# Performance work log

Measured on AMD Instinct MI355X. Metric: run time of the kernel, lower is better.

## Reference

```python
import jax, jax.numpy as jnp
import numpy as np

N = 20000      # nodes
E = 640000     # edges (before self-loops)
NFEAT = 512
NHID = 128
HEADS = 2
NOUT = 64
K = 100
ALPHA = 0.2          # LeakyReLU negative slope
CLUSTER_TEMP = 5.0


def gat_layer(x, W, a_src, a_dst, b, src, dst, n, heads, out_c, neg_slope):
    """PyG-style GATConv (eval mode, self-loops already in src/dst).
    W: [heads*out_c, in_c], a_src/a_dst: [heads, out_c], b: [heads*out_c]."""
    h = (x @ W.T).reshape(n, heads, out_c)               # [N,H,C]
    alpha_src = (h * a_src[None]).sum(-1)                # [N,H]
    alpha_dst = (h * a_dst[None]).sum(-1)                # [N,H]
    e = alpha_src[src] + alpha_dst[dst]                  # [E',H]
    e = jnp.where(e > 0, e, neg_slope * e)               # LeakyReLU
    # segment softmax over incoming edges of each dst node
    m = jax.ops.segment_max(e, dst, num_segments=n)
    ex = jnp.exp(e - m[dst])
    s = jax.ops.segment_sum(ex, dst, num_segments=n)
    a = ex / (s[dst] + 1e-16)                            # [E',H]
    out = jax.ops.segment_sum(h[src] * a[:, :, None], dst, num_segments=n)
    return out.reshape(n, heads * out_c) + b


def cluster_iter(data_n, mu, num_iter, cluster_temp):
    """Soft k-means on row-normalized data. data_n: [N,D], mu: [K,D]."""
    def body(mu, _):
        dist = data_n @ mu.T                              # [N,K]
        r = jax.nn.softmax(cluster_temp * dist, axis=1)
        cluster_r = r.sum(axis=0)                         # [K]
        cluster_mean = r.T @ data_n                       # [K,D]
        return cluster_mean / cluster_r[:, None], None
    mu, _ = jax.lax.scan(body, mu, None, length=num_iter)
    dist = data_n @ mu.T
    r = jax.nn.softmax(cluster_temp * dist, axis=1)
    return mu, r, dist


def setup_inputs() -> dict:
    key = jax.random.key(0)
    ks = jax.random.split(key, 12)
    x = jax.random.normal(ks[0], (N, NFEAT), dtype=jnp.float32)
    edge_index = jax.random.randint(ks[1], (2, E), 0, N, dtype=jnp.int32)
    # GATConv layer 1 params
    W1 = jax.random.normal(ks[2], (HEADS * NHID, NFEAT), dtype=jnp.float32) * 0.05
    a_src1 = jax.random.normal(ks[3], (HEADS, NHID), dtype=jnp.float32) * 0.1
    a_dst1 = jax.random.normal(ks[4], (HEADS, NHID), dtype=jnp.float32) * 0.1
    b1 = jnp.zeros((HEADS * NHID,), dtype=jnp.float32)
    # GATConv layer 2 params (heads=1)
    W2 = jax.random.normal(ks[5], (NOUT, HEADS * NHID), dtype=jnp.float32) * 0.05
    a_src2 = jax.random.normal(ks[6], (1, NOUT), dtype=jnp.float32) * 0.1
    a_dst2 = jax.random.normal(ks[7], (1, NOUT), dtype=jnp.float32) * 0.1
    b2 = jnp.zeros((NOUT,), dtype=jnp.float32)
    # cluster init (self.init = torch.rand(K, nout))
    mu0 = jax.random.uniform(ks[8], (K, NOUT), dtype=jnp.float32)
    return {"x": x, "W1": W1, "a_src1": a_src1, "a_dst1": a_dst1, "b1": b1,
            "W2": W2, "a_src2": a_src2, "a_dst2": a_dst2, "b2": b2,
            "mu0": mu0, "edge_index": edge_index, "num_iter": 10}


def reference(x, W1, a_src1, a_dst1, b1, W2, a_src2, a_dst2, b2, mu0,
              edge_index, num_iter):
    loops = jnp.arange(N, dtype=edge_index.dtype)
    src = jnp.concatenate([edge_index[0], loops])
    dst = jnp.concatenate([edge_index[1], loops])
    h = jax.nn.elu(gat_layer(x, W1, a_src1, a_dst1, b1, src, dst,
                             N, HEADS, NHID, ALPHA))
    embeds = gat_layer(h, W2, a_src2, a_dst2, b2, src, dst,
                       N, 1, NOUT, ALPHA) + 1e-6
    data_n = embeds / jnp.linalg.norm(embeds, axis=1, keepdims=True)
    mu_init, _, _ = cluster_iter(data_n, mu0, num_iter, CLUSTER_TEMP)
    mu, r, dist = cluster_iter(data_n, jax.lax.stop_gradient(mu_init), 1,
                               CLUSTER_TEMP)
    return mu, r, embeds, dist
```

## Files before the change

kernel.cpp:

```cpp
#include <hip/hip_runtime.h>
#include <hip/hip_bf16.h>
#include <math.h>

#define Nn 20000
#define Ee 640000
#define ETOT 660000
#define NF 512
#define C1 256
#define C2 64
#define KC 100
#define TEMP 5.0f
#define NSLOPE 0.2f
#define NPB 500
#define CHB 40

typedef __attribute__((ext_vector_type(8))) short bf16x8;
typedef __attribute__((ext_vector_type(4))) float f32x4;

__device__ __forceinline__ float wredSum(float v) {
#pragma unroll
  for (int off = 32; off > 0; off >>= 1) v += __shfl_xor(v, off, 64);
  return v;
}
__device__ __forceinline__ ushort f2bf(float f) {
  __hip_bfloat16 b = __float2bfloat16(f);
  return *(ushort*)&b;
}
__device__ __forceinline__ float bf2f(ushort u) {
  __hip_bfloat16 b = *(__hip_bfloat16*)&u;
  return __bfloat162float(b);
}

__global__ void hist_kernel(const int* __restrict__ ei, int* __restrict__ deg) {
  int e = blockIdx.x * 256 + threadIdx.x;
  if (e >= ETOT) return;
  int dst = e < Ee ? ei[Ee + e] : e - Ee;
  atomicAdd(&deg[dst], 1);
}

__global__ __launch_bounds__(1024) void scan2_kernel(const int* __restrict__ deg,
    int* __restrict__ rowp, int* __restrict__ curs) {
  __shared__ int wsum[16];
  __shared__ int wpre[16];
  int t = threadIdx.x;
  int lane = t & 63, w = t >> 6;
  int loc[20];
  int tot = 0;
  int base = t * 20;
  if (t < 1000) {
#pragma unroll
    for (int i = 0; i < 20; i++) { tot += deg[base + i]; loc[i] = tot; }
  }
  int s = tot;
#pragma unroll
  for (int off = 1; off < 64; off <<= 1) {
    int u = __shfl_up(s, off, 64);
    if (lane >= off) s += u;
  }
  if (lane == 63) wsum[w] = s;
  __syncthreads();
  if (t == 0) {
    int c = 0;
#pragma unroll
    for (int i = 0; i < 16; i++) { c += wsum[i]; wpre[i] = c; }
    rowp[0] = 0;
  }
  __syncthreads();
  int p = (w > 0 ? wpre[w - 1] : 0) + s - tot;
  if (t < 1000) {
    int prev = 0;
#pragma unroll
    for (int i = 0; i < 20; i++) {
      rowp[base + i + 1] = p + loc[i];
      curs[base + i] = p + prev;
      prev = loc[i];
    }
  }
}

__global__ void scatter_kernel(const int* __restrict__ ei, int* __restrict__ curs,
                               int* __restrict__ ssort, int* __restrict__ dsort) {
  int e = blockIdx.x * 256 + threadIdx.x;
  if (e >= ETOT) return;
  int src = e < Ee ? ei[e] : e - Ee;
  int dst = e < Ee ? ei[Ee + e] : e - Ee;
  int pos = atomicAdd(&curs[dst], 1);
  ssort[pos] = src;
  dsort[pos] = dst;
}

__global__ __launch_bounds__(256) void edge_e1(const int* __restrict__ ssort,
    const int* __restrict__ dsort, const float* __restrict__ asn,
    const float* __restrict__ adn, float2* __restrict__ eb) {
  int i = blockIdx.x * 256 + threadIdx.x;
  if (i >= ETOT) return;
  int s = ssort[i], d = dsort[i];
  float2 a = ((const float2*)asn)[s];
  float2 b = ((const float2*)adn)[d];
  float e0 = a.x + b.x, e1 = a.y + b.y;
  e0 = e0 > 0.f ? e0 : NSLOPE * e0;
  e1 = e1 > 0.f ? e1 : NSLOPE * e1;
  eb[i] = make_float2(e0, e1);
}

__global__ __launch_bounds__(256) void edge_e2(const int* __restrict__ ssort,
    const int* __restrict__ dsort, const float* __restrict__ asn,
    const float* __restrict__ adn, float* __restrict__ eb) {
  int i = blockIdx.x * 256 + threadIdx.x;
  if (i >= ETOT) return;
  float e = asn[ssort[i]] + adn[dsort[i]];
  eb[i] = e > 0.f ? e : NSLOPE * e;
}

__global__ __launch_bounds__(256) void gemm1_mfma(const float* __restrict__ A,
    const float* __restrict__ B, float* __restrict__ C) {
  __shared__ ushort Ah[128 * 40], Al[128 * 40], Bh[128 * 40], Bl[128 * 40];
  int tid = threadIdx.x;
  int bm = blockIdx.x << 7, bn = blockIdx.y << 7;
  int w = tid >> 6, lane = tid & 63;
  int wm = (w >> 1) << 6, wn = (w & 1) << 6;
  int fr = lane & 15, ko = (lane >> 4) << 3;
  f32x4 acc[4][4] = {};
  for (int k0 = 0; k0 < 512; k0 += 32) {
    __syncthreads();
#pragma unroll
    for (int cc = 0; cc < 4; cc++) {
      int c = tid + (cc << 8);
      int row = c >> 3, q = c & 7;
      int off = row * 40 + (q << 2);
      int gr = bm + row;
      float4 va = (gr < Nn) ? *(const float4*)(A + (size_t)gr * NF + k0 + (q << 2))
                            : make_float4(0.f, 0.f, 0.f, 0.f);
      float4 vb = *(const float4*)(B + (size_t)(bn + row) * NF + k0 + (q << 2));
      ushort h0 = f2bf(va.x), h1 = f2bf(va.y), h2 = f2bf(va.z), h3 = f2bf(va.w);
      *(ushort4*)&Ah[off] = make_ushort4(h0, h1, h2, h3);
      *(ushort4*)&Al[off] = make_ushort4(
          f2bf(va.x - bf2f(h0)), f2bf(va.y - bf2f(h1)),
          f2bf(va.z - bf2f(h2)), f2bf(va.w - bf2f(h3)));
      ushort g0 = f2bf(vb.x), g1 = f2bf(vb.y), g2 = f2bf(vb.z), g3 = f2bf(vb.w);
      *(ushort4*)&Bh[off] = make_ushort4(g0, g1, g2, g3);
      *(ushort4*)&Bl[off] = make_ushort4(
          f2bf(vb.x - bf2f(g0)), f2bf(vb.y - bf2f(g1)),
          f2bf(vb.z - bf2f(g2)), f2bf(vb.w - bf2f(g3)));
    }
    __syncthreads();
    bf16x8 aH[4], bH[4], t[4];
#pragma unroll
    for (int mf = 0; mf < 4; mf++)
      aH[mf] = *(const bf16x8*)&Ah[(wm + (mf << 4) + fr) * 40 + ko];
#pragma unroll
    for (int nf = 0; nf < 4; nf++)
      bH[nf] = *(const bf16x8*)&Bh[(wn + (nf << 4) + fr) * 40 + ko];
#pragma unroll
    for (int mf = 0; mf < 4; mf++)
#pragma unroll
      for (int nf = 0; nf < 4; nf++)
        acc[mf][nf] = __builtin_amdgcn_mfma_f32_16x16x32_bf16(aH[mf], bH[nf], acc[mf][nf], 0, 0, 0);
#pragma unroll
    for (int nf = 0; nf < 4; nf++)
      t[nf] = *(const bf16x8*)&Bl[(wn + (nf << 4) + fr) * 40 + ko];
#pragma unroll
    for (int mf = 0; mf < 4; mf++)
#pragma unroll
      for (int nf = 0; nf < 4; nf++)
        acc[mf][nf] = __builtin_amdgcn_mfma_f32_16x16x32_bf16(aH[mf], t[nf], acc[mf][nf], 0, 0, 0);
#pragma unroll
    for (int mf = 0; mf < 4; mf++)
      t[mf] = *(const bf16x8*)&Al[(wm + (mf << 4) + fr) * 40 + ko];
#pragma unroll
    for (int mf = 0; mf < 4; mf++)
#pragma unroll
      for (int nf = 0; nf < 4; nf++)
        acc[mf][nf] = __builtin_amdgcn_mfma_f32_16x16x32_bf16(t[mf], bH[nf], acc[mf][nf], 0, 0, 0);
  }
  int cr = (lane >> 4) << 2, cc2 = lane & 15;
#pragma unroll
  for (int mf = 0; mf < 4; mf++) {
#pragma unroll
    for (int r = 0; r < 4; r++) {
      int row = bm + wm + (mf << 4) + cr + r;
      if (row < Nn) {
#pragma unroll
        for (int nf = 0; nf < 4; nf++)
          C[(size_t)row * C1 + bn + wn + (nf << 4) + cc2] = acc[mf][nf][r];
      }
    }
  }
}

__global__ __launch_bounds__(256) void gemm_nt(const float* __restrict__ A,
    const float* __restrict__ B, float* __restrict__ C, int M, int N, int K) {
  __shared__ __align__(16) float As[16][68];
  __shared__ __align__(16) float Bs[16][68];
  int tid = threadIdx.x;
  int bm = blockIdx.x << 6, bn = blockIdx.y << 6;
  int lr = tid >> 2;
  int lc = (tid & 3) << 2;
  int tx = tid & 15, ty = tid >> 4;
  float acc[4][4] = {};
  for (int k0 = 0; k0 < K; k0 += 16) {
    int am = bm + lr;
    float4 av = make_float4(0.f, 0.f, 0.f, 0.f);
    if (am < M) av = *(const float4*)(A + (size_t)am * K + k0 + lc);
    float4 bv = *(const float4*)(B + (size_t)(bn + lr) * K + k0 + lc);
    __syncthreads();
    As[lc + 0][lr] = av.x; As[lc + 1][lr] = av.y; As[lc + 2][lr] = av.z; As[lc + 3][lr] = av.w;
    Bs[lc + 0][lr] = bv.x; Bs[lc + 1][lr] = bv.y; Bs[lc + 2][lr] = bv.z; Bs[lc + 3][lr] = bv.w;
    __syncthreads();
#pragma unroll
    for (int k = 0; k < 16; k++) {
      float4 a = *(const float4*)&As[k][ty << 2];
      float4 b = *(const float4*)&Bs[k][tx << 2];
      float aa[4] = {a.x, a.y, a.z, a.w};
      float bb[4] = {b.x, b.y, b.z, b.w};
#pragma unroll
      for (int i = 0; i < 4; i++)
#pragma unroll
        for (int j = 0; j < 4; j++) acc[i][j] += aa[i] * bb[j];
    }
  }
#pragma unroll
  for (int i = 0; i < 4; i++) {
    int row = bm + (ty << 2) + i;
    if (row < M) {
#pragma unroll
      for (int j = 0; j < 4; j++)
        C[(size_t)row * N + bn + (tx << 2) + j] = acc[i][j];
    }
  }
}

__global__ __launch_bounds__(256) void alpha1_kernel(const float* __restrict__ h,
    const float* __restrict__ a_src, const float* __restrict__ a_dst,
    float* __restrict__ asn, float* __restrict__ adn) {
  int l = threadIdx.x & 63;
  int n = (blockIdx.x << 2) + (threadIdx.x >> 6);
  if (n >= Nn) return;
  const float* hr = h + (size_t)n * C1;
  float h0 = hr[l], h1v = hr[64 + l], h2v = hr[128 + l], h3v = hr[192 + l];
  float ps0 = h0 * a_src[l] + h1v * a_src[64 + l];
  float pd0 = h0 * a_dst[l] + h1v * a_dst[64 + l];
  float ps1 = h2v * a_src[128 + l] + h3v * a_src[192 + l];
  float pd1 = h2v * a_dst[128 + l] + h3v * a_dst[192 + l];
  ps0 = wredSum(ps0); pd0 = wredSum(pd0); ps1 = wredSum(ps1); pd1 = wredSum(pd1);
  if (l == 0) {
    asn[2 * n] = ps0; asn[2 * n + 1] = ps1;
    adn[2 * n] = pd0; adn[2 * n + 1] = pd1;
  }
}

__global__ __launch_bounds__(256) void alpha2_kernel(const float* __restrict__ h,
    const float* __restrict__ a_src, const float* __restrict__ a_dst,
    float* __restrict__ asn, float* __restrict__ adn) {
  int l = threadIdx.x & 63;
  int n = (blockIdx.x << 2) + (threadIdx.x >> 6);
  if (n >= Nn) return;
  float v = h[(size_t)n * C2 + l];
  float ps = wredSum(v * a_src[l]);
  float pd = wredSum(v * a_dst[l]);
  if (l == 0) { asn[n] = ps; adn[n] = pd; }
}

__global__ __launch_bounds__(256) void agg1_kernel(const float* __restrict__ h,
    const float2* __restrict__ eb, const int* __restrict__ ssort,
    const float* __restrict__ b1, const int* __restrict__ rowp,
    float* __restrict__ ho) {
  __shared__ float redm[8], reds[8];
  __shared__ __align__(16) float slab[4][256];
  int n = blockIdx.x, tid = threadIdx.x;
  int w = tid >> 6, l = tid & 63;
  int lo = rowp[n], hi = rowp[n + 1];
  float m0 = -1e30f, s0 = 0.f, m1 = -1e30f, s1 = 0.f;
  for (int i = lo + tid; i < hi; i += 256) {
    float2 e = eb[i];
    if (e.x > m0) { s0 = s0 * __expf(m0 - e.x) + 1.f; m0 = e.x; }
    else s0 += __expf(e.x - m0);
    if (e.y > m1) { s1 = s1 * __expf(m1 - e.y) + 1.f; m1 = e.y; }
    else s1 += __expf(e.y - m1);
  }
#pragma unroll
  for (int off = 32; off > 0; off >>= 1) {
    float om = __shfl_xor(m0, off, 64), os = __shfl_xor(s0, off, 64);
    float nm = fmaxf(m0, om);
    s0 = s0 * __expf(m0 - nm) + os * __expf(om - nm); m0 = nm;
    om = __shfl_xor(m1, off, 64); os = __shfl_xor(s1, off, 64);
    nm = fmaxf(m1, om);
    s1 = s1 * __expf(m1 - nm) + os * __expf(om - nm); m1 = nm;
  }
  if (l == 0) { redm[w] = m0; reds[w] = s0; redm[4 + w] = m1; reds[4 + w] = s1; }
  __syncthreads();
  float M0 = fmaxf(fmaxf(redm[0], redm[1]), fmaxf(redm[2], redm[3]));
  float M1 = fmaxf(fmaxf(redm[4], redm[5]), fmaxf(redm[6], redm[7]));
  float S0 = reds[0] * __expf(redm[0] - M0) + reds[1] * __expf(redm[1] - M0)
           + reds[2] * __expf(redm[2] - M0) + reds[3] * __expf(redm[3] - M0);
  float S1 = reds[4] * __expf(redm[4] - M1) + reds[5] * __expf(redm[5] - M1)
           + reds[6] * __expf(redm[6] - M1) + reds[7] * __expf(redm[7] - M1);
  float inv0 = 1.f / (S0 + 1e-16f), inv1 = 1.f / (S1 + 1e-16f);
  const bool lo_head = (l < 32);
  float Msel = lo_head ? M0 : M1;
  float isel = lo_head ? inv0 : inv1;
  int ch = l << 2;
  int deg = hi - lo;
  float4 accA = {0.f, 0.f, 0.f, 0.f}, accB = {0.f, 0.f, 0.f, 0.f};
  int j = w;
  for (; j + 4 < deg; j += 8) {
    int i0 = lo + j, i1 = lo + j + 4;
    float2 eA = eb[i0];
    float2 eB = eb[i1];
    int sA = ssort[i0], sB = ssort[i1];
    float4 ha = *(const float4*)(h + (size_t)sA * C1 + ch);
    float4 hb = *(const float4*)(h + (size_t)sB * C1 + ch);
    float wtA = __expf((lo_head ? eA.x : eA.y) - Msel) * isel;
    float wtB = __expf((lo_head ? eB.x : eB.y) - Msel) * isel;
    accA.x += wtA * ha.x; accA.y += wtA * ha.y; accA.z += wtA * ha.z; accA.w += wtA * ha.w;
    accB.x += wtB * hb.x; accB.y += wtB * hb.y; accB.z += wtB * hb.z; accB.w += wtB * hb.w;
  }
  if (j < deg) {
    int i0 = lo + j;
    float2 eA = eb[i0];
    int sA = ssort[i0];
    float4 ha = *(const float4*)(h + (size_t)sA * C1 + ch);
    float wtA = __expf((lo_head ? eA.x : eA.y) - Msel) * isel;
    accA.x += wtA * ha.x; accA.y += wtA * ha.y; accA.z += wtA * ha.z; accA.w += wtA * ha.w;
  }
  accA.x += accB.x; accA.y += accB.y; accA.z += accB.z; accA.w += accB.w;
  *(float4*)&slab[w][ch] = accA;
  __syncthreads();
  float v = slab[0][tid] + slab[1][tid] + slab[2][tid] + slab[3][tid] + b1[tid];
  ho[(size_t)n * C1 + tid] = v > 0.f ? v : __expf(v) - 1.0f;
}

__global__ __launch_bounds__(256) void agg2_kernel(const float* __restrict__ h,
    const float* __restrict__ eb, const int* __restrict__ ssort,
    const float* __restrict__ b2, const int* __restrict__ rowp,
    float* __restrict__ emb, float* __restrict__ dnrm) {
  int tid = threadIdx.x;
  int w = tid >> 6, l = tid & 63;
  int n = (blockIdx.x << 2) + w;
  int lo = rowp[n], hi = rowp[n + 1];
  float m = -1e30f, s = 0.f;
  for (int i = lo + l; i < hi; i += 64) {
    float e = eb[i];
    if (e > m) { s = s * __expf(m - e) + 1.f; m = e; }
    else s += __expf(e - m);
  }
#pragma unroll
  for (int off = 32; off > 0; off >>= 1) {
    float om = __shfl_xor(m, off, 64), os = __shfl_xor(s, off, 64);
    float nm = fmaxf(m, om);
    s = s * __expf(m - nm) + os * __expf(om - nm); m = nm;
  }
  float inv = 1.f / (s + 1e-16f);
  int g = l >> 4, lg = l & 15, ch = lg << 2;
  int deg = hi - lo;
  float4 accA = {0.f, 0.f, 0.f, 0.f}, accB = {0.f, 0.f, 0.f, 0.f};
  int j = g;
  for (; j + 4 < deg; j += 8) {
    int i0 = lo + j, i1 = lo + j + 4;
    float eA = eb[i0], eB = eb[i1];
    int sA = ssort[i0], sB = ssort[i1];
    float4 ha = *(const float4*)(h + (size_t)sA * C2 + ch);
    float4 hb = *(const float4*)(h + (size_t)sB * C2 + ch);
    float wtA = __expf(eA - m) * inv;
    float wtB = __expf(eB - m) * inv;
    accA.x += wtA * ha.x; accA.y += wtA * ha.y; accA.z += wtA * ha.z; accA.w += wtA * ha.w;
    accB.x += wtB * hb.x; accB.y += wtB * hb.y; accB.z += wtB * hb.z; accB.w += wtB * hb.w;
  }
  if (j < deg) {
    int i0 = lo + j;
    float eA = eb[i0];
    int sA = ssort[i0];
    float4 ha = *(const float4*)(h + (size_t)sA * C2 + ch);
    float wtA = __expf(eA - m) * inv;
    accA.x += wtA * ha.x; accA.y += wtA * ha.y; accA.z += wtA * ha.z; accA.w += wtA * ha.w;
  }
  accA.x += accB.x; accA.y += accB.y; accA.z += accB.z; accA.w += accB.w;
#pragma unroll
  for (int off = 16; off <= 32; off <<= 1) {
    accA.x += __shfl_xor(accA.x, off, 64);
    accA.y += __shfl_xor(accA.y, off, 64);
    accA.z += __shfl_xor(accA.z, off, 64);
    accA.w += __shfl_xor(accA.w, off, 64);
  }
  float4 bv = *(const float4*)(b2 + ch);
  float e0 = accA.x + bv.x + 1e-6f;
  float e1 = accA.y + bv.y + 1e-6f;
  float e2 = accA.z + bv.z + 1e-6f;
  float e3 = accA.w + bv.w + 1e-6f;
  float dot = e0 * e0 + e1 * e1 + e2 * e2 + e3 * e3;
#pragma unroll
  for (int off = 1; off < 16; off <<= 1) dot += __shfl_xor(dot, off, 64);
  float invn = 1.f / sqrtf(dot);
  if (g == 0) {
    *(float4*)(emb + (size_t)n * C2 + ch) = make_float4(e0, e1, e2, e3);
    *(float4*)(dnrm + (size_t)n * C2 + ch) =
        make_float4(e0 * invn, e1 * invn, e2 * invn, e3 * invn);
  }
}

template <int MODE>
__global__ __launch_bounds__(256) void fused_ac(
    const float* __restrict__ dnp, const float* __restrict__ mu_init,
    const float* __restrict__ mu, float* __restrict__ pcm, float* __restrict__ pcr,
    float* __restrict__ rout, float* __restrict__ distout,
    int it, const int* __restrict__ niter) {
  if (MODE == 0) { if (it > niter[0]) return; }
  __shared__ __align__(16) float mu_s[KC * 68];
  __shared__ __align__(16) float d_s[CHB * 64];
  __shared__ __align__(16) float r_s[CHB * KC];
  int tid = threadIdx.x, blk = blockIdx.x;
  const float* msrc = (MODE == 0 && it == 0) ? mu_init : mu;
  for (int idx = tid; idx < KC * 64; idx += 256)
    mu_s[(idx >> 6) * 68 + (idx & 63)] = msrc[idx];
  for (int idx = tid; idx < CHB * 64; idx += 256)
    d_s[idx] = dnp[(size_t)blk * (CHB * 64) + idx];
  __syncthreads();
  int w = tid >> 6, l = tid & 63;
  const bool has2 = l < (KC - 64);
  int l2 = has2 ? 64 + l : l;
  int nbase = w * 10;
  float z1[5][2] = {}, z2[5][2] = {};
#pragma unroll 4
  for (int dq = 0; dq < 16; dq++) {
    float4 m1 = *(const float4*)&mu_s[l * 68 + (dq << 2)];
    float4 m2 = *(const float4*)&mu_s[l2 * 68 + (dq << 2)];
#pragma unroll
    for (int g = 0; g < 5; g++) {
#pragma unroll
      for (int nb = 0; nb < 2; nb++) {
        float4 dv = *(const float4*)&d_s[(nbase + g * 2 + nb) * 64 + (dq << 2)];
        z1[g][nb] += m1.x * dv.x + m1.y * dv.y + m1.z * dv.z + m1.w * dv.w;
        z2[g][nb] += m2.x * dv.x + m2.y * dv.y + m2.z * dv.z + m2.w * dv.w;
      }
    }
  }
#pragma unroll
  for (int g = 0; g < 5; g++) {
#pragma unroll
    for (int nb = 0; nb < 2; nb++) {
      float e1 = __expf(TEMP * z1[g][nb]);
      float e2 = has2 ? __expf(TEMP * z2[g][nb]) : 0.f;
      float inv = 1.0f / wredSum(e1 + e2);
      int nl = nbase + g * 2 + nb;
      if (MODE == 0) {
        r_s[nl * KC + l] = e1 * inv;
        if (has2) r_s[nl * KC + 64 + l] = e2 * inv;
      } else {
        size_t n = (size_t)blk * CHB + nl;
        rout[n * KC + l] = e1 * inv;
        if (has2) rout[n * KC + 64 + l] = e2 * inv;
        distout[n * KC + l] = z1[g][nb];
        if (has2) distout[n * KC + 64 + l] = z2[g][nb];
      }
    }
  }
  if (MODE == 0) {
    __syncthreads();
    int tx = tid & 15, ky = tid >> 4;
    const bool two = (ky < 9);
    int kq0 = ky, kq1 = 16 + ky;
    float a0[4][4] = {}, a1[4][4] = {};
    float ar0[4] = {}, ar1[4] = {};
#pragma unroll 2
    for (int j = 0; j < CHB; j++) {
      float4 dv = *(const float4*)&d_s[j * 64 + (tx << 2)];
      float4 r0 = *(const float4*)&r_s[j * KC + (kq0 << 2)];
      float rv0[4] = {r0.x, r0.y, r0.z, r0.w};
#pragma unroll
      for (int i = 0; i < 4; i++) {
        a0[i][0] += rv0[i] * dv.x; a0[i][1] += rv0[i] * dv.y;
        a0[i][2] += rv0[i] * dv.z; a0[i][3] += rv0[i] * dv.w;
      }
      if (tx == 0) { ar0[0] += r0.x; ar0[1] += r0.y; ar0[2] += r0.z; ar0[3] += r0.w; }
      if (two) {
        float4 r1 = *(const float4*)&r_s[j * KC + (kq1 << 2)];
        float rv1[4] = {r1.x, r1.y, r1.z, r1.w};
#pragma unroll
        for (int i = 0; i < 4; i++) {
          a1[i][0] += rv1[i] * dv.x; a1[i][1] += rv1[i] * dv.y;
          a1[i][2] += rv1[i] * dv.z; a1[i][3] += rv1[i] * dv.w;
        }
        if (tx == 0) { ar1[0] += r1.x; ar1[1] += r1.y; ar1[2] += r1.z; ar1[3] += r1.w; }
      }
    }
#pragma unroll
    for (int i = 0; i < 4; i++) {
      *(float4*)&pcm[(size_t)blk * 6400 + (kq0 * 4 + i) * 64 + (tx << 2)] =
          make_float4(a0[i][0], a0[i][1], a0[i][2], a0[i][3]);
      if (two)
        *(float4*)&pcm[(size_t)blk * 6400 + (kq1 * 4 + i) * 64 + (tx << 2)] =
            make_float4(a1[i][0], a1[i][1], a1[i][2], a1[i][3]);
    }
    if (tx == 0) {
      *(float4*)&pcr[(size_t)blk * KC + kq0 * 4] = make_float4(ar0[0], ar0[1], ar0[2], ar0[3]);
      if (two)
        *(float4*)&pcr[(size_t)blk * KC + kq1 * 4] = make_float4(ar1[0], ar1[1], ar1[2], ar1[3]);
    }
  }
}

__global__ __launch_bounds__(256) void muupd_kernel(const float* __restrict__ pcm,
    const float* __restrict__ pcr, float* __restrict__ mu,
    int it, const int* __restrict__ niter) {
  if (it > niter[0]) return;
  __shared__ float part[4][64];
  __shared__ float redc[4];
  int k = blockIdx.x, tid = threadIdx.x;
  int d = tid & 63, bg = tid >> 6;
  float s = 0.f;
  for (int b = bg; b < NPB; b += 4)
    s += pcm[(size_t)b * 6400 + k * 64 + d];
  part[bg][d] = s;
  float c = 0.f;
  for (int b = tid; b < NPB; b += 256) c += pcr[b * KC + k];
  c = wredSum(c);
  if ((tid & 63) == 0) redc[tid >> 6] = c;
  __syncthreads();
  if (tid < 64) {
    float cr = redc[0] + redc[1] + redc[2] + redc[3];
    mu[k * 64 + tid] = (part[0][tid] + part[1][tid] + part[2][tid] + part[3][tid]) / cr;
  }
}

__global__ void copy_f(const float* __restrict__ a, float* __restrict__ b, int n) {
  int i = blockIdx.x * 256 + threadIdx.x;
  if (i < n) b[i] = a[i];
}

extern "C" void kernel_launch(void* const* d_in, const int* in_sizes, int n_in,
                              void* d_out, int out_size, void* d_ws, size_t ws_size,
                              hipStream_t stream) {
  const float* x    = (const float*)d_in[0];
  const float* W1   = (const float*)d_in[1];
  const float* asr1 = (const float*)d_in[2];
  const float* ads1 = (const float*)d_in[3];
  const float* b1   = (const float*)d_in[4];
  const float* W2   = (const float*)d_in[5];
  const float* asr2 = (const float*)d_in[6];
  const float* ads2 = (const float*)d_in[7];
  const float* b2   = (const float*)d_in[8];
  const float* mu0  = (const float*)d_in[9];
  const int*   ei   = (const int*)d_in[10];
  const int*   nit  = (const int*)d_in[11];

  float* f = (float*)d_ws;
  float* h1   = f;  f += (size_t)Nn * C1;
  float* h1o  = f;  f += (size_t)Nn * C1;
  float* as1  = f;  f += Nn * 2;
  float* ad1  = f;  f += Nn * 2;
  float* h2   = f;  f += (size_t)Nn * C2;
  float* as2  = f;  f += Nn;
  float* ad2  = f;  f += Nn;
  float* dn   = f;  f += (size_t)Nn * C2;
  float* mu   = f;  f += KC * C2;
  float2* ebA = (float2*)f; f += (size_t)ETOT * 2;
  float* ebB  = (float*)ebA;
  float* pcm  = h1;
  float* pcr  = h1 + (size_t)NPB * 6400;
  int* ip = (int*)f;
  int* deg   = ip;  ip += Nn;
  int* rowp  = ip;  ip += Nn + 1;
  int* curs  = ip;  ip += Nn;
  int* ssort = ip;  ip += ETOT;
  int* dsort = ip;  ip += ETOT;

  float* out_mu = (float*)d_out;
  float* out_r  = out_mu + KC * C2;
  float* out_e  = out_r + (size_t)Nn * KC;
  float* out_d  = out_e + (size_t)Nn * C2;

  hipMemsetAsync(deg, 0, Nn * sizeof(int), stream);
  hist_kernel<<<(ETOT + 255) / 256, 256, 0, stream>>>(ei, deg);
  scan2_kernel<<<1, 1024, 0, stream>>>(deg, rowp, curs);
  scatter_kernel<<<(ETOT + 255) / 256, 256, 0, stream>>>(ei, curs, ssort, dsort);

  gemm1_mfma<<<dim3(157, 2), 256, 0, stream>>>(x, W1, h1);
  alpha1_kernel<<<5000, 256, 0, stream>>>(h1, asr1, ads1, as1, ad1);
  edge_e1<<<(ETOT + 255) / 256, 256, 0, stream>>>(ssort, dsort, as1, ad1, ebA);
  agg1_kernel<<<Nn, 256, 0, stream>>>(h1, ebA, ssort, b1, rowp, h1o);

  gemm_nt<<<dim3(313, 1), 256, 0, stream>>>(h1o, W2, h2, Nn, C2, C1);
  alpha2_kernel<<<5000, 256, 0, stream>>>(h2, asr2, ads2, as2, ad2);
  edge_e2<<<(ETOT + 255) / 256, 256, 0, stream>>>(ssort, dsort, as2, ad2, ebB);
  agg2_kernel<<<5000, 256, 0, stream>>>(h2, ebB, ssort, b2, rowp, out_e, dn);

  for (int it = 0; it < 12; it++) {
    fused_ac<0><<<NPB, 256, 0, stream>>>(dn, mu0, mu, pcm, pcr, nullptr, nullptr, it, nit);
    muupd_kernel<<<KC, 256, 0, stream>>>(pcm, pcr, mu, it, nit);
  }
  fused_ac<1><<<NPB, 256, 0, stream>>>(dn, mu0, mu, nullptr, nullptr, out_r, out_d, 0, nit);
  copy_f<<<25, 256, 0, stream>>>(mu, out_mu, KC * C2);
}
```

Measured before the change: 1.053 ms.

## Replace per-block partials and mu-update kernel with atomic accumulation slabs

Each k-means iteration block now atomically adds its partial cluster sums and counts into a per-iteration slab, instead of writing them to a partial buffer that a separate muupd kernel reduces. The next iteration's kernel normalizes the previous slab while loading mu, so the 12 muupd launches and the final copy kernel are removed. This cuts launch count and the partial-buffer write and reread. In exchange, it adds heavy float atomic contention (500 blocks each adding 6400 values), a memset of the slabs, and a summation order that is no longer deterministic.

```diff
diff --git a/kernel.cpp b/kernel.cpp
--- a/kernel.cpp
+++ b/kernel.cpp
@@ -13,6 +13,7 @@
 #define NSLOPE 0.2f
 #define NPB 500
 #define CHB 40
+#define SLAB 6500
 
 typedef __attribute__((ext_vector_type(8))) short bf16x8;
 typedef __attribute__((ext_vector_type(4))) float f32x4;
@@ -401,17 +402,26 @@
 template <int MODE>
 __global__ __launch_bounds__(256) void fused_ac(
     const float* __restrict__ dnp, const float* __restrict__ mu_init,
-    const float* __restrict__ mu, float* __restrict__ pcm, float* __restrict__ pcr,
-    float* __restrict__ rout, float* __restrict__ distout,
+    float* __restrict__ muacc,
+    float* __restrict__ rout, float* __restrict__ distout, float* __restrict__ out_mu,
     int it, const int* __restrict__ niter) {
   if (MODE == 0) { if (it > niter[0]) return; }
   __shared__ __align__(16) float mu_s[KC * 68];
   __shared__ __align__(16) float d_s[CHB * 64];
   __shared__ __align__(16) float r_s[CHB * KC];
+  __shared__ float rcp_s[KC];
   int tid = threadIdx.x, blk = blockIdx.x;
-  const float* msrc = (MODE == 0 && it == 0) ? mu_init : mu;
-  for (int idx = tid; idx < KC * 64; idx += 256)
-    mu_s[(idx >> 6) * 68 + (idx & 63)] = msrc[idx];
+  int src_it = (MODE == 0) ? it - 1 : niter[0];
+  if (MODE == 0 && it == 0) {
+    for (int idx = tid; idx < KC * 64; idx += 256)
+      mu_s[(idx >> 6) * 68 + (idx & 63)] = mu_init[idx];
+  } else {
+    const float* acc_prev = muacc + (size_t)src_it * SLAB;
+    if (tid < KC) rcp_s[tid] = 1.0f / acc_prev[6400 + tid];
+    __syncthreads();
+    for (int idx = tid; idx < KC * 64; idx += 256)
+      mu_s[(idx >> 6) * 68 + (idx & 63)] = acc_prev[idx] * rcp_s[idx >> 6];
+  }
   for (int idx = tid; idx < CHB * 64; idx += 256)
     d_s[idx] = dnp[(size_t)blk * (CHB * 64) + idx];
   __syncthreads();
@@ -456,6 +466,7 @@
   }
   if (MODE == 0) {
     __syncthreads();
+    float* acc = muacc + (size_t)it * SLAB;
     int tx = tid & 15, ky = tid >> 4;
     const bool two = (ky < 9);
     int kq0 = ky, kq1 = 16 + ky;
@@ -485,46 +496,25 @@
     }
 #pragma unroll
     for (int i = 0; i < 4; i++) {
-      *(float4*)&pcm[(size_t)blk * 6400 + (kq0 * 4 + i) * 64 + (tx << 2)] =
-          make_float4(a0[i][0], a0[i][1], a0[i][2], a0[i][3]);
-      if (two)
-        *(float4*)&pcm[(size_t)blk * 6400 + (kq1 * 4 + i) * 64 + (tx << 2)] =
-            make_float4(a1[i][0], a1[i][1], a1[i][2], a1[i][3]);
+#pragma unroll
+      for (int q = 0; q < 4; q++) {
+        atomicAdd(&acc[(kq0 * 4 + i) * 64 + (tx << 2) + q], a0[i][q]);
+        if (two) atomicAdd(&acc[(kq1 * 4 + i) * 64 + (tx << 2) + q], a1[i][q]);
+      }
     }
     if (tx == 0) {
-      *(float4*)&pcr[(size_t)blk * KC + kq0 * 4] = make_float4(ar0[0], ar0[1], ar0[2], ar0[3]);
-      if (two)
-        *(float4*)&pcr[(size_t)blk * KC + kq1 * 4] = make_float4(ar1[0], ar1[1], ar1[2], ar1[3]);
-    }
-  }
-}
-
-__global__ __launch_bounds__(256) void muupd_kernel(const float* __restrict__ pcm,
-    const float* __restrict__ pcr, float* __restrict__ mu,
-    int it, const int* __restrict__ niter) {
-  if (it > niter[0]) return;
-  __shared__ float part[4][64];
-  __shared__ float redc[4];
-  int k = blockIdx.x, tid = threadIdx.x;
-  int d = tid & 63, bg = tid >> 6;
-  float s = 0.f;
-  for (int b = bg; b < NPB; b += 4)
-    s += pcm[(size_t)b * 6400 + k * 64 + d];
-  part[bg][d] = s;
-  float c = 0.f;
-  for (int b = tid; b < NPB; b += 256) c += pcr[b * KC + k];
-  c = wredSum(c);
-  if ((tid & 63) == 0) redc[tid >> 6] = c;
-  __syncthreads();
-  if (tid < 64) {
-    float cr = redc[0] + redc[1] + redc[2] + redc[3];
-    mu[k * 64 + tid] = (part[0][tid] + part[1][tid] + part[2][tid] + part[3][tid]) / cr;
-  }
-}
-
-__global__ void copy_f(const float* __restrict__ a, float* __restrict__ b, int n) {
-  int i = blockIdx.x * 256 + threadIdx.x;
-  if (i < n) b[i] = a[i];
+#pragma unroll
+      for (int i = 0; i < 4; i++) {
+        atomicAdd(&acc[6400 + kq0 * 4 + i], ar0[i]);
+        if (two) atomicAdd(&acc[6400 + kq1 * 4 + i], ar1[i]);
+      }
+    }
+  } else {
+    if (blk == 0) {
+      for (int idx = tid; idx < KC * 64; idx += 256)
+        out_mu[idx] = mu_s[(idx >> 6) * 68 + (idx & 63)];
+    }
+  }
 }
 
 extern "C" void kernel_launch(void* const* d_in, const int* in_sizes, int n_in,
@@ -544,19 +534,17 @@
   const int*   nit  = (const int*)d_in[11];
 
   float* f = (float*)d_ws;
-  float* h1   = f;  f += (size_t)Nn * C1;
-  float* h1o  = f;  f += (size_t)Nn * C1;
-  float* as1  = f;  f += Nn * 2;
-  float* ad1  = f;  f += Nn * 2;
-  float* h2   = f;  f += (size_t)Nn * C2;
-  float* as2  = f;  f += Nn;
-  float* ad2  = f;  f += Nn;
-  float* dn   = f;  f += (size_t)Nn * C2;
-  float* mu   = f;  f += KC * C2;
+  float* h1    = f;  f += (size_t)Nn * C1;
+  float* h1o   = f;  f += (size_t)Nn * C1;
+  float* as1   = f;  f += Nn * 2;
+  float* ad1   = f;  f += Nn * 2;
+  float* h2    = f;  f += (size_t)Nn * C2;
+  float* as2   = f;  f += Nn;
+  float* ad2   = f;  f += Nn;
+  float* dn    = f;  f += (size_t)Nn * C2;
+  float* muacc = f;  f += (size_t)12 * SLAB;
   float2* ebA = (float2*)f; f += (size_t)ETOT * 2;
   float* ebB  = (float*)ebA;
-  float* pcm  = h1;
-  float* pcr  = h1 + (size_t)NPB * 6400;
   int* ip = (int*)f;
   int* deg   = ip;  ip += Nn;
   int* rowp  = ip;  ip += Nn + 1;
@@ -570,6 +558,7 @@
   float* out_d  = out_e + (size_t)Nn * C2;
 
   hipMemsetAsync(deg, 0, Nn * sizeof(int), stream);
+  hipMemsetAsync(muacc, 0, (size_t)12 * SLAB * sizeof(float), stream);
   hist_kernel<<<(ETOT + 255) / 256, 256, 0, stream>>>(ei, deg);
   scan2_kernel<<<1, 1024, 0, stream>>>(deg, rowp, curs);
   scatter_kernel<<<(ETOT + 255) / 256, 256, 0, stream>>>(ei, curs, ssort, dsort);
@@ -584,10 +573,7 @@
   edge_e2<<<(ETOT + 255) / 256, 256, 0, stream>>>(ssort, dsort, as2, ad2, ebB);
   agg2_kernel<<<5000, 256, 0, stream>>>(h2, ebB, ssort, b2, rowp, out_e, dn);
 
-  for (int it = 0; it < 12; it++) {
-    fused_ac<0><<<NPB, 256, 0, stream>>>(dn, mu0, mu, pcm, pcr, nullptr, nullptr, it, nit);
-    muupd_kernel<<<KC, 256, 0, stream>>>(pcm, pcr, mu, it, nit);
-  }
-  fused_ac<1><<<NPB, 256, 0, stream>>>(dn, mu0, mu, nullptr, nullptr, out_r, out_d, 0, nit);
-  copy_f<<<25, 256, 0, stream>>>(mu, out_mu, KC * C2);
-}
+  for (int it = 0; it < 12; it++)
+    fused_ac<0><<<NPB, 256, 0, stream>>>(dn, mu0, muacc, nullptr, nullptr, nullptr, it, nit);
+  fused_ac<1><<<NPB, 256, 0, stream>>>(dn, mu0, muacc, out_r, out_d, out_mu, 0, nit);
+}
```

After: 2.046 ms. 1.94x slower.
